# Performance work log

Measured on AMD Instinct MI355X. Metric: run time of the kernel, lower is better.

Reference implementation:

```python
import jax, jax.numpy as jnp
import numpy as np

H = 1152        # hidden_size
NH = 16         # num_heads
HD = H // NH    # head_dim = 72
MLP = int(H * 4.0)
EPS = 1e-6


def _ln(z, scale=None):
    # LayerNorm over last axis, eps=1e-6, no bias
    m = jnp.mean(z, axis=-1, keepdims=True)
    v = jnp.mean(jnp.square(z - m), axis=-1, keepdims=True)
    y = (z - m) * jax.lax.rsqrt(v + EPS)
    if scale is not None:
        y = y * scale
    return y


def setup_inputs() -> dict:
    key = jax.random.key(0)
    ks = jax.random.split(key, 16)
    B, N = 16, 1024
    x = jax.random.normal(ks[0], (B, N, H), dtype=jnp.float32)
    c = jax.random.normal(ks[1], (B, H), dtype=jnp.float32)
    def xav(k, fan_in, fan_out):
        lim = np.sqrt(6.0 / (fan_in + fan_out))
        return jax.random.uniform(k, (fan_in, fan_out), jnp.float32, -lim, lim)
    # adaLN modulation Dense (zero-init in original; use small random for a non-trivial test)
    w_mod = 0.02 * jax.random.normal(ks[2], (H, 6 * H), dtype=jnp.float32)
    b_mod = 0.02 * jax.random.normal(ks[3], (6 * H,), dtype=jnp.float32)
    w_qkv = xav(ks[4], H, 3 * H)
    b_qkv = jnp.zeros((3 * H,), jnp.float32)
    g_q = jnp.ones((HD,), jnp.float32)
    g_k = jnp.ones((HD,), jnp.float32)
    w_proj = xav(ks[5], H, H)
    b_proj = jnp.zeros((H,), jnp.float32)
    w1 = xav(ks[6], H, MLP)
    b1 = jnp.zeros((MLP,), jnp.float32)
    w2 = xav(ks[7], MLP, H)
    b2 = jnp.zeros((H,), jnp.float32)
    return dict(x=x, c=c, w_mod=w_mod, b_mod=b_mod, w_qkv=w_qkv, b_qkv=b_qkv,
                g_q=g_q, g_k=g_k, w_proj=w_proj, b_proj=b_proj,
                w1=w1, b1=b1, w2=w2, b2=b2)


def reference(x, c, w_mod, b_mod, w_qkv, b_qkv, g_q, g_k, w_proj, b_proj, w1, b1, w2, b2):
    B, N, _ = x.shape
    # adaLN-zero modulation from conditioning
    mod = jax.nn.swish(c) @ w_mod + b_mod                    # (B, 6H)
    sh_msa, sc_msa, g_msa, sh_mlp, sc_mlp, g_mlp = jnp.split(mod, 6, axis=1)
    # --- attention branch ---
    xn = _ln(x) * (1 + sc_msa[:, None, :]) + sh_msa[:, None, :]
    qkv = xn @ w_qkv + b_qkv                                 # (B, N, 3H)
    qkv = qkv.reshape(B, N, 3, NH, HD).transpose(2, 0, 3, 1, 4)
    q, k, v = qkv[0], qkv[1], qkv[2]                         # (B, NH, N, HD)
    q = _ln(q, g_q)
    k = _ln(k, g_k)
    attn = jax.nn.softmax(jnp.einsum('bhqd,bhkd->bhqk', q, k) * (HD ** -0.5), axis=-1)
    o = jnp.einsum('bhqk,bhkd->bhqd', attn, v)
    o = o.transpose(0, 2, 1, 3).reshape(B, N, H) @ w_proj + b_proj
    x = x + g_msa[:, None, :] * o
    # --- MLP branch ---
    xn2 = _ln(x) * (1 + sc_mlp[:, None, :]) + sh_mlp[:, None, :]
    h = jax.nn.gelu(xn2 @ w1 + b1, approximate=True)
    x = x + g_mlp[:, None, :] * (h @ w2 + b2)
    return x
```

## Files before the change

kernel.cpp:

```cpp
#include <hip/hip_runtime.h>
#include <hip/hip_bf16.h>

#define H     1152
#define H3    3456
#define H6    6912
#define NTOK  1024
#define NB    16
#define NHEAD 16
#define HDIM  72
#define MLPD  4608
#define ROWS  (NB*NTOK)
#define KSPLIT 16

typedef __hip_bfloat16 bf16;
typedef float f32x4 __attribute__((ext_vector_type(4)));
typedef __bf16 bf16x8 __attribute__((ext_vector_type(8)));
typedef const __attribute__((address_space(1))) void* gptr_as1;
typedef __attribute__((address_space(3))) void* lptr_as3;

__device__ __forceinline__ float b2f(bf16 v){ return __bfloat162float(v); }
__device__ __forceinline__ bf16  f2b(float v){ return __float2bfloat16(v); }
__device__ __forceinline__ unsigned short f2bu(float v){ return __builtin_bit_cast(unsigned short, __float2bfloat16(v)); }

template<int CTRL>
__device__ __forceinline__ float fdpp(float x) {
    int xi = __float_as_int(x);
    int r = __builtin_amdgcn_update_dpp(xi, xi, CTRL, 0xF, 0xF, true);
    return __int_as_float(r);
}
__device__ __forceinline__ float rowmax16(float x) {
    x = fmaxf(x, fdpp<0xB1>(x));
    x = fmaxf(x, fdpp<0x4E>(x));
    x = fmaxf(x, fdpp<0x141>(x));
    x = fmaxf(x, fdpp<0x140>(x));
    return x;
}
__device__ __forceinline__ float rowsum16(float x) {
    x += fdpp<0xB1>(x);
    x += fdpp<0x4E>(x);
    x += fdpp<0x141>(x);
    x += fdpp<0x140>(x);
    return x;
}

__global__ __launch_bounds__(256) void mod_partial_kernel(const float* __restrict__ c,
                                                          const float* __restrict__ w_mod,
                                                          float* __restrict__ partial) {
    const int ks = blockIdx.y;
    const int k0 = ks * (H/KSPLIT);
    __shared__ float sw[NB*(H/KSPLIT)];
    for (int i = threadIdx.x; i < NB*(H/KSPLIT); i += 256) {
        int b = i/(H/KSPLIT), k = i - b*(H/KSPLIT);
        float cv = c[b*H + k0 + k];
        sw[i] = cv / (1.f + __expf(-cv));
    }
    __syncthreads();
    const int col = blockIdx.x*256 + threadIdx.x;
    float acc[NB];
    #pragma unroll
    for (int b = 0; b < NB; ++b) acc[b] = 0.f;
    for (int k = 0; k < H/KSPLIT; ++k) {
        float wv = w_mod[(long)(k0+k)*H6 + col];
        #pragma unroll
        for (int b = 0; b < NB; ++b) acc[b] += sw[b*(H/KSPLIT)+k] * wv;
    }
    #pragma unroll
    for (int b = 0; b < NB; ++b) partial[((long)ks*NB + b)*H6 + col] = acc[b];
}

__global__ __launch_bounds__(256) void mod_reduce_kernel(const float* __restrict__ partial,
                                                         const float* __restrict__ b_mod,
                                                         float* __restrict__ mod) {
    const int idx = blockIdx.x*256 + threadIdx.x;
    const int col = idx % H6;
    float s = b_mod[col];
    #pragma unroll
    for (int ks = 0; ks < KSPLIT; ++ks) s += partial[(long)ks*NB*H6 + idx];
    mod[idx] = s;
}

__global__ __launch_bounds__(256) void ln_mod_kernel(const float* __restrict__ xin,
                                                     const float* __restrict__ mod,
                                                     int sh_off, int sc_off,
                                                     bf16* __restrict__ out,
                                                     int row0) {
    const int lrow = blockIdx.x;
    const long grow = (long)row0 + lrow;
    const int b = (int)(grow >> 10);
    const int tid = threadIdx.x;
    const long ibase = grow * H;
    const long obase = (long)lrow * H;
    __shared__ float sred[8];
    float vals[5];
    float sum = 0.f, sq = 0.f;
    #pragma unroll
    for (int i = 0; i < 5; ++i) {
        int cidx = i*256 + tid;
        float v = 0.f;
        if (cidx < H) v = xin[ibase+cidx];
        vals[i] = v; sum += v; sq += v*v;
    }
    #pragma unroll
    for (int off = 32; off > 0; off >>= 1) { sum += __shfl_down(sum, off); sq += __shfl_down(sq, off); }
    int wave = tid >> 6, lane = tid & 63;
    if (lane == 0) { sred[wave] = sum; sred[4+wave] = sq; }
    __syncthreads();
    if (tid == 0) {
        sred[0] = sred[0]+sred[1]+sred[2]+sred[3];
        sred[4] = sred[4]+sred[5]+sred[6]+sred[7];
    }
    __syncthreads();
    float mean = sred[0] * (1.f/H);
    float var  = sred[4] * (1.f/H) - mean*mean;
    float rstd = rsqrtf(var + 1e-6f);
    const float* mrow = mod + b*H6;
    #pragma unroll
    for (int i = 0; i < 5; ++i) {
        int cidx = i*256 + tid;
        if (cidx < H) {
            float y = (vals[i]-mean)*rstd;
            out[obase+cidx] = f2b(y * (1.f + mrow[sc_off+cidx]) + mrow[sh_off+cidx]);
        }
    }
}

__global__ __launch_bounds__(256) void transpose_kernel(const float* __restrict__ in,
                                                        bf16* __restrict__ out, int R, int C) {
    __shared__ bf16 tile[32][33];
    int c0 = blockIdx.x*32, r0 = blockIdx.y*32;
    int tx = threadIdx.x & 31, ty = threadIdx.x >> 5;
    for (int j = ty; j < 32; j += 8) tile[j][tx] = f2b(in[(long)(r0+j)*C + c0 + tx]);
    __syncthreads();
    for (int j = ty; j < 32; j += 8) out[(long)(c0+j)*R + r0 + tx] = tile[tx][j];
}

template<int EPI>
__global__ __launch_bounds__(256) void gemm_bt(const bf16* __restrict__ A, const bf16* __restrict__ BT,
                                               const float* __restrict__ bias,
                                               const float* __restrict__ res, const float* __restrict__ gate,
                                               bf16* __restrict__ C, float* __restrict__ Cf,
                                               int M, int N, int K, int row0) {
    __shared__ __align__(16) bf16 As[128*64];
    __shared__ __align__(16) bf16 Bs[128*64];
    const int tid  = threadIdx.x;
    const int wave = tid >> 6, lane = tid & 63;
    const int wm = wave & 1, wn = wave >> 1;
    const int col = lane & 15, quad = lane >> 4;
    f32x4 acc[4][4];
    #pragma unroll
    for (int i = 0; i < 4; ++i)
        #pragma unroll
        for (int j = 0; j < 4; ++j) acc[i][j] = (f32x4){0.f,0.f,0.f,0.f};

    const long arow0 = (long)blockIdx.y * 128;
    const long brow0 = (long)blockIdx.x * 128;
    const int  srow  = tid >> 3;
    const int  scol  = (tid & 7) * 8;
    const bf16* Ag = A + (arow0 + srow)*(long)K + scol;
    const bf16* Bg = BT + (brow0 + srow)*(long)K + scol;
    bf16* Asl = As + tid*8;
    bf16* Bsl = Bs + tid*8;

    for (int k0 = 0; k0 < K; k0 += 64) {
        __syncthreads();
        #pragma unroll
        for (int i = 0; i < 4; ++i) {
            __builtin_amdgcn_global_load_lds((gptr_as1)(Ag + (long)i*32*K + k0), (lptr_as3)(Asl + i*2048), 16, 0, 0);
            __builtin_amdgcn_global_load_lds((gptr_as1)(Bg + (long)i*32*K + k0), (lptr_as3)(Bsl + i*2048), 16, 0, 0);
        }
        __syncthreads();
        #pragma unroll
        for (int kk = 0; kk < 64; kk += 32) {
            bf16x8 af[4], bfr[4];
            #pragma unroll
            for (int mt = 0; mt < 4; ++mt) af[mt]  = *(const bf16x8*)&As[(wm*64+mt*16+col)*64 + kk + quad*8];
            #pragma unroll
            for (int nt = 0; nt < 4; ++nt) bfr[nt] = *(const bf16x8*)&Bs[(wn*64+nt*16+col)*64 + kk + quad*8];
            #pragma unroll
            for (int mt = 0; mt < 4; ++mt)
                #pragma unroll
                for (int nt = 0; nt < 4; ++nt)
                    acc[mt][nt] = __builtin_amdgcn_mfma_f32_16x16x32_bf16(af[mt], bfr[nt], acc[mt][nt], 0, 0, 0);
        }
    }

    #pragma unroll
    for (int mt = 0; mt < 4; ++mt) {
        #pragma unroll
        for (int nt = 0; nt < 4; ++nt) {
            const int colg = (int)brow0 + wn*64 + nt*16 + col;
            const float bv = bias[colg];
            #pragma unroll
            for (int r = 0; r < 4; ++r) {
                const long rowg = arow0 + wm*64 + mt*16 + quad*4 + r;
                float v = acc[mt][nt][r] + bv;
                if (EPI == 1) {
                    float u = 0.7978845608028654f*(v + 0.044715f*v*v*v);
                    v = v / (1.f + exp2f(-2.885390081777927f*u));
                    C[rowg*(long)N + colg] = f2b(v);
                } else if (EPI == 2) {
                    const long grow = row0 + rowg;
                    float g = gate[(int)(grow>>10)*H6 + colg];
                    Cf[grow*(long)N + colg] = res[grow*(long)N + colg] + g*v;
                } else {
                    C[rowg*(long)N + colg] = f2b(v);
                }
            }
        }
    }
}

__device__ __forceinline__ void ln72q(const bf16* __restrict__ src, const float* __restrict__ gw,
                                      float scale, bf16* __restrict__ dst, int lane) {
    const int i1 = 64 + (lane & 7);
    float e0 = b2f(src[lane]);
    float e1 = (lane < 8) ? b2f(src[i1]) : 0.f;
    float s = e0 + e1;
    #pragma unroll
    for (int off = 32; off > 0; off >>= 1) s += __shfl_xor(s, off);
    float mean = s * (1.f/72.f);
    float d0 = e0 - mean;
    float d1 = (lane < 8) ? (e1 - mean) : 0.f;
    float sq = d0*d0 + d1*d1;
    #pragma unroll
    for (int off = 32; off > 0; off >>= 1) sq += __shfl_xor(sq, off);
    float rstd = rsqrtf(sq*(1.f/72.f) + 1e-6f);
    dst[lane] = f2b(d0*rstd*gw[lane]*scale);
    if (lane < 32) {
        float y1 = (lane < 8) ? d1*rstd*gw[i1]*scale : 0.f;
        dst[64+lane] = f2b(y1);
    }
}

__device__ __forceinline__ void ln72k(const bf16* __restrict__ src, const float* __restrict__ gw,
                                      bf16* __restrict__ kb, int n, int lane) {
    const int i1 = 64 + (lane & 7);
    float e0 = b2f(src[lane]);
    float e1 = (lane < 8) ? b2f(src[i1]) : 0.f;
    float s = e0 + e1;
    #pragma unroll
    for (int off = 32; off > 0; off >>= 1) s += __shfl_xor(s, off);
    float mean = s * (1.f/72.f);
    float d0 = e0 - mean;
    float d1 = (lane < 8) ? (e1 - mean) : 0.f;
    float sq = d0*d0 + d1*d1;
    #pragma unroll
    for (int off = 32; off > 0; off >>= 1) sq += __shfl_xor(sq, off);
    float rstd = rsqrtf(sq*(1.f/72.f) + 1e-6f);
    const int kvb = n >> 4, nc = n & 15;
    {
        int off1 = ((kvb*3 + (lane>>5))<<9) + ((((lane&31)>>3)<<4) + nc)*8 + (lane&7);
        kb[off1] = f2b(d0*rstd*gw[lane]);
    }
    if (lane < 32) {
        float y1 = (lane < 8) ? d1*rstd*gw[i1] : 0.f;
        int off2 = ((kvb*3 + 2)<<9) + (((lane>>3)<<4) + nc)*8 + (lane&7);
        kb[off2] = f2b(y1);
    }
}

__global__ __launch_bounds__(256) void qk_ln_kernel(const bf16* __restrict__ qkv,
                                                    const float* __restrict__ g_q, const float* __restrict__ g_k,
                                                    bf16* __restrict__ qln, bf16* __restrict__ kln) {
    const int wave = threadIdx.x >> 6, lane = threadIdx.x & 63;
    const long g  = (long)blockIdx.x*4 + wave;
    const int  n  = (int)(g & 1023);
    const long bh = g >> 10;
    const int  h  = (int)(bh & 15);
    const int  b  = (int)(bh >> 4);
    const bf16* src = qkv + ((long)b*NTOK + n)*H3 + h*HDIM;
    ln72q(src,     g_q, 0.11785113019775793f * 1.4426950408889634f, qln + (bh*NTOK + n)*96, lane);
    ln72k(src + H, g_k, kln + bh*98304, n, lane);
}

__global__ __launch_bounds__(256) void v_transpose_kernel(const bf16* __restrict__ qkv, bf16* __restrict__ vt) {
    const int n0 = blockIdx.x*64;
    const int h = blockIdx.y, b = blockIdx.z;
    __shared__ bf16 tile[64][80];
    const long srcbase = ((long)b*NTOK + n0)*H3 + 2*H + h*HDIM;
    for (int idx = threadIdx.x; idx < 64*72; idx += 256) {
        int n = idx/72, d = idx - n*72;
        tile[n][d] = qkv[srcbase + (long)n*H3 + d];
    }
    for (int idx = threadIdx.x; idx < 64*8; idx += 256) {
        int n = idx >> 3, d = idx & 7;
        tile[n][72+d] = f2b(0.f);
    }
    __syncthreads();
    const long bh = (long)(b*NHEAD + h);
    bf16* dst = vt + (bh*16 + blockIdx.x)*5120;
    for (int o = threadIdx.x; o < 5120; o += 256) {
        int hv5 = o >> 9;
        int hv = (hv5 >= 5) ? 1 : 0;
        int nt = hv5 - hv*5;
        int lane = (o >> 3) & 63;
        int e = o & 7;
        int pos = hv*32 + ((lane>>4)<<3) + e;
        int kv_local = ((pos & 3) << 4) + (pos >> 2);
        int d = (nt << 4) + (lane & 15);
        dst[o] = tile[kv_local][d];
        (void)nt;
    }
}

#define PSTR 72
__global__ __launch_bounds__(512) void attn_kernel(const bf16* __restrict__ qln, const bf16* __restrict__ kln,
                                                   const bf16* __restrict__ vt, bf16* __restrict__ o,
                                                   int Bc) {
    const int tid = threadIdx.x;
    const int wave = tid >> 6, lane = tid & 63;
    const int qg = wave & 3, half = wave >> 2;
    const int col = lane & 15, quad = lane >> 4;

    const int L = blockIdx.x;
    const int P_ = 2*Bc;
    const int c8 = L & 7;
    const int j  = L >> 3;
    const int bh_l = c8*P_ + (j % P_);
    const int qt   = j / P_;
    const int b = bh_l >> 4, h = bh_l & 15;
    const long bh = bh_l;

    const int q0 = qt*64 + qg*16;
    const bf16* qb = qln + bh*NTOK*96;
    const bf16* kb = kln + bh*98304;
    const bf16* vb = vt  + bh*81920;

    __shared__ __align__(16) char smraw[28672];
    bf16* pw = (bf16*)smraw + wave*(16*PSTR);
    f32x4* Osm = (f32x4*)smraw;
    f32x4* Msm = (f32x4*)(smraw + 20480);
    f32x4* Lsm = (f32x4*)(smraw + 24576);

    bf16x8 qf[3];
    #pragma unroll
    for (int ks = 0; ks < 3; ++ks) qf[ks] = *(const bf16x8*)&qb[(q0+col)*96 + ks*32 + quad*8];

    f32x4 oacc[5];
    #pragma unroll
    for (int i = 0; i < 5; ++i) oacc[i] = (f32x4){0.f,0.f,0.f,0.f};
    float mrow[4], lrow[4];
    #pragma unroll
    for (int r = 0; r < 4; ++r) { mrow[r] = -1e30f; lrow[r] = 0.f; }

    const int kvbeg = half*512, kvend = kvbeg + 512;
    for (int kv0 = kvbeg; kv0 < kvend; kv0 += 64) {
        const int kvb16 = kv0 >> 4;
        const int kvt   = kv0 >> 6;
        f32x4 s[4];
        #pragma unroll
        for (int j4 = 0; j4 < 4; ++j4) s[j4] = (f32x4){0.f,0.f,0.f,0.f};
        #pragma unroll
        for (int j4 = 0; j4 < 4; ++j4)
            #pragma unroll
            for (int ks = 0; ks < 3; ++ks) {
                bf16x8 kf = *(const bf16x8*)&kb[(((kvb16 + j4)*3 + ks)<<9) + lane*8];
                s[j4] = __builtin_amdgcn_mfma_f32_16x16x32_bf16(qf[ks], kf, s[j4], 0, 0, 0);
            }
        float alpha[4];
        #pragma unroll
        for (int r = 0; r < 4; ++r) {
            float tm = fmaxf(fmaxf(s[0][r], s[1][r]), fmaxf(s[2][r], s[3][r]));
            tm = rowmax16(tm);
            float mn = fmaxf(mrow[r], tm);
            alpha[r] = exp2f(mrow[r] - mn);
            float p0 = exp2f(s[0][r] - mn);
            float p1 = exp2f(s[1][r] - mn);
            float p2 = exp2f(s[2][r] - mn);
            float p3 = exp2f(s[3][r] - mn);
            float ts = rowsum16((p0+p1)+(p2+p3));
            lrow[r] = lrow[r]*alpha[r] + ts;
            mrow[r] = mn;
            const int prow = quad*4 + r;
            unsigned int lo = (unsigned int)f2bu(p0) | ((unsigned int)f2bu(p1) << 16);
            unsigned int hi = (unsigned int)f2bu(p2) | ((unsigned int)f2bu(p3) << 16);
            unsigned long long pk = (unsigned long long)lo | ((unsigned long long)hi << 32);
            *(unsigned long long*)&pw[prow*PSTR + col*4] = pk;
        }
        if (__any(alpha[0]+alpha[1]+alpha[2]+alpha[3] < 4.f)) {
            #pragma unroll
            for (int i = 0; i < 5; ++i)
                #pragma unroll
                for (int r = 0; r < 4; ++r) oacc[i][r] *= alpha[r];
        }
        bf16x8 pf0 = *(const bf16x8*)&pw[col*PSTR + quad*8];
        bf16x8 pf1 = *(const bf16x8*)&pw[col*PSTR + 32 + quad*8];
        #pragma unroll
        for (int nt = 0; nt < 5; ++nt) {
            bf16x8 vf0 = *(const bf16x8*)&vb[((kvt*10 + nt)<<9) + lane*8];
            bf16x8 vf1 = *(const bf16x8*)&vb[((kvt*10 + 5 + nt)<<9) + lane*8];
            oacc[nt] = __builtin_amdgcn_mfma_f32_16x16x32_bf16(pf0, vf0, oacc[nt], 0, 0, 0);
            oacc[nt] = __builtin_amdgcn_mfma_f32_16x16x32_bf16(pf1, vf1, oacc[nt], 0, 0, 0);
        }
    }

    __syncthreads();
    if (half) {
        f32x4 mv, lv;
        #pragma unroll
        for (int r = 0; r < 4; ++r) { mv[r] = mrow[r]; lv[r] = lrow[r]; }
        Msm[qg*64 + lane] = mv;
        Lsm[qg*64 + lane] = lv;
        #pragma unroll
        for (int nt = 0; nt < 5; ++nt) Osm[(qg*5 + nt)*64 + lane] = oacc[nt];
    }
    __syncthreads();
    if (!half) {
        f32x4 mB = Msm[qg*64 + lane];
        f32x4 lB = Lsm[qg*64 + lane];
        float aA[4], aB[4], inv[4];
        #pragma unroll
        for (int r = 0; r < 4; ++r) {
            float ms = fmaxf(mrow[r], mB[r]);
            aA[r] = exp2f(mrow[r] - ms);
            aB[r] = exp2f(mB[r] - ms);
            float ls = lrow[r]*aA[r] + lB[r]*aB[r];
            inv[r] = 1.f / ls;
        }
        #pragma unroll
        for (int nt = 0; nt < 5; ++nt) {
            f32x4 oB = Osm[(qg*5 + nt)*64 + lane];
            int d = nt*16 + col;
            if (d < HDIM) {
                #pragma unroll
                for (int r = 0; r < 4; ++r) {
                    int qrow = q0 + quad*4 + r;
                    o[((long)b*NTOK + qrow)*H + h*HDIM + d] = f2b((oacc[nt][r]*aA[r] + oB[r]*aB[r])*inv[r]);
                }
            }
        }
    }
}

extern "C" void kernel_launch(void* const* d_in, const int* in_sizes, int n_in,
                              void* d_out, int out_size, void* d_ws, size_t ws_size,
                              hipStream_t stream) {
    const float* x      = (const float*)d_in[0];
    const float* c      = (const float*)d_in[1];
    const float* w_mod  = (const float*)d_in[2];
    const float* b_mod  = (const float*)d_in[3];
    const float* w_qkv  = (const float*)d_in[4];
    const float* b_qkv  = (const float*)d_in[5];
    const float* g_q    = (const float*)d_in[6];
    const float* g_k    = (const float*)d_in[7];
    const float* w_proj = (const float*)d_in[8];
    const float* b_proj = (const float*)d_in[9];
    const float* w1     = (const float*)d_in[10];
    const float* b1     = (const float*)d_in[11];
    const float* w2     = (const float*)d_in[12];
    const float* b2     = (const float*)d_in[13];
    float* out = (float*)d_out;

    char* ws = (char*)d_ws;
    size_t off = 0;
    auto alloc = [&](size_t bytes) { void* p = ws + off; off += (bytes + 255) & ~(size_t)255; return p; };
    float* modb  = (float*)alloc((size_t)NB*H6*4);
    bf16* wqkvT  = (bf16*)alloc((size_t)H3*H*2);
    bf16* wprojT = (bf16*)alloc((size_t)H*H*2);
    bf16* w1T    = (bf16*)alloc((size_t)MLPD*H*2);
    bf16* w2T    = (bf16*)alloc((size_t)H*MLPD*2);
    const size_t pers = off;

    int nchunk = 4;
    while (nchunk < 16 && pers + (size_t)(ROWS/nchunk)*(9216+8704) > ws_size) nchunk <<= 1;
    const int Rc = ROWS / nchunk;
    const int Bc = NB / nchunk;

    char* R1 = ws + pers;
    char* R2 = R1 + (size_t)Rc*9216;
    bf16* qkvc = (bf16*)R1;
    bf16* oc   = (bf16*)R1;
    bf16* hc   = (bf16*)R1;
    bf16* xnc  = (bf16*)R2;
    bf16* qlnc = (bf16*)R2;
    bf16* klnc = (bf16*)(R2 + (size_t)Rc*3072);
    bf16* vtc  = (bf16*)(R2 + (size_t)Rc*6144);
    float* modp = (float*)R1;

    mod_partial_kernel<<<dim3(H6/256, KSPLIT), 256, 0, stream>>>(c, w_mod, modp);
    mod_reduce_kernel<<<dim3(NB*H6/256), 256, 0, stream>>>(modp, b_mod, modb);
    transpose_kernel<<<dim3(H3/32,  H/32),   256, 0, stream>>>(w_qkv,  wqkvT,  H,    H3);
    transpose_kernel<<<dim3(H/32,   H/32),   256, 0, stream>>>(w_proj, wprojT, H,    H);
    transpose_kernel<<<dim3(MLPD/32,H/32),   256, 0, stream>>>(w1,     w1T,    H,    MLPD);
    transpose_kernel<<<dim3(H/32,   MLPD/32),256, 0, stream>>>(w2,     w2T,    MLPD, H);

    for (int ci = 0; ci < nchunk; ++ci) {
        const int row0 = ci * Rc;
        ln_mod_kernel<<<dim3(Rc), 256, 0, stream>>>(x, modb, 0, H, xnc, row0);
        gemm_bt<0><<<dim3(H3/128, Rc/128), 256, 0, stream>>>(xnc, wqkvT, b_qkv, nullptr, nullptr, qkvc, nullptr, Rc, H3, H, 0);
        qk_ln_kernel<<<dim3(Bc*NHEAD*NTOK/4), 256, 0, stream>>>(qkvc, g_q, g_k, qlnc, klnc);
        v_transpose_kernel<<<dim3(NTOK/64, NHEAD, Bc), 256, 0, stream>>>(qkvc, vtc);
        attn_kernel<<<dim3(256*Bc), 512, 0, stream>>>(qlnc, klnc, vtc, oc, Bc);
        gemm_bt<2><<<dim3(H/128, Rc/128), 256, 0, stream>>>(oc, wprojT, b_proj, x, modb + 2*H, nullptr, out, Rc, H, H, row0);
        ln_mod_kernel<<<dim3(Rc), 256, 0, stream>>>(out, modb, 3*H, 4*H, xnc, row0);
        gemm_bt<1><<<dim3(MLPD/128, Rc/128), 256, 0, stream>>>(xnc, w1T, b1, nullptr, nullptr, hc, nullptr, Rc, MLPD, H, 0);
        gemm_bt<2><<<dim3(H/128, Rc/128), 256, 0, stream>>>(hc, w2T, b2, out, modb + 5*H, nullptr, out, Rc, H, MLPD, row0);
    }
}
```

Before: 1.880 ms.

## Swizzle GEMM LDS tiles, remap blocks across XCDs, and default to one chunk

The GEMM now reads global memory with an XOR-swizzled column offset so that LDS fragment reads avoid bank conflicts. It also launches a 1D grid that is remapped so consecutive tiles are grouped per XCD (when the block count is a multiple of 8), which should improve L2 reuse. The attention block-index mapping is simplified to fixed shifts, and the chunk count now starts at 1, so the whole batch runs per launch when the workspace is large enough. Processing the batch in one pass needs a much larger workspace, and the fixed attention mapping assumes the per-chunk layout divides cleanly.

```diff
diff --git a/kernel.cpp b/kernel.cpp
--- a/kernel.cpp
+++ b/kernel.cpp
@@ -146,18 +146,26 @@
     const int wave = tid >> 6, lane = tid & 63;
     const int wm = wave & 1, wn = wave >> 1;
     const int col = lane & 15, quad = lane >> 4;
+
+    const int nbx = N >> 7;
+    const int nwg = gridDim.x;
+    const int L = blockIdx.x;
+    const int l = ((nwg & 7) == 0) ? ((L & 7)*(nwg >> 3) + (L >> 3)) : L;
+    const int bx = l % nbx, by = l / nbx;
+
     f32x4 acc[4][4];
     #pragma unroll
     for (int i = 0; i < 4; ++i)
         #pragma unroll
         for (int j = 0; j < 4; ++j) acc[i][j] = (f32x4){0.f,0.f,0.f,0.f};
 
-    const long arow0 = (long)blockIdx.y * 128;
-    const long brow0 = (long)blockIdx.x * 128;
+    const long arow0 = (long)by * 128;
+    const long brow0 = (long)bx * 128;
     const int  srow  = tid >> 3;
     const int  scol  = (tid & 7) * 8;
-    const bf16* Ag = A + (arow0 + srow)*(long)K + scol;
-    const bf16* Bg = BT + (brow0 + srow)*(long)K + scol;
+    const int  scolsw = scol ^ ((srow & 7) * 8);
+    const bf16* Ag = A + (arow0 + srow)*(long)K + scolsw;
+    const bf16* Bg = BT + (brow0 + srow)*(long)K + scolsw;
     bf16* Asl = As + tid*8;
     bf16* Bsl = Bs + tid*8;
 
@@ -169,13 +177,14 @@
             __builtin_amdgcn_global_load_lds((gptr_as1)(Bg + (long)i*32*K + k0), (lptr_as3)(Bsl + i*2048), 16, 0, 0);
         }
         __syncthreads();
+        const int xr = (col & 7) * 8;
         #pragma unroll
         for (int kk = 0; kk < 64; kk += 32) {
             bf16x8 af[4], bfr[4];
             #pragma unroll
-            for (int mt = 0; mt < 4; ++mt) af[mt]  = *(const bf16x8*)&As[(wm*64+mt*16+col)*64 + kk + quad*8];
+            for (int mt = 0; mt < 4; ++mt) af[mt]  = *(const bf16x8*)&As[(wm*64+mt*16+col)*64 + ((kk + quad*8) ^ xr)];
             #pragma unroll
-            for (int nt = 0; nt < 4; ++nt) bfr[nt] = *(const bf16x8*)&Bs[(wn*64+nt*16+col)*64 + kk + quad*8];
+            for (int nt = 0; nt < 4; ++nt) bfr[nt] = *(const bf16x8*)&Bs[(wn*64+nt*16+col)*64 + ((kk + quad*8) ^ xr)];
             #pragma unroll
             for (int mt = 0; mt < 4; ++mt)
                 #pragma unroll
@@ -313,11 +322,11 @@
     const int col = lane & 15, quad = lane >> 4;
 
     const int L = blockIdx.x;
-    const int P_ = 2*Bc;
     const int c8 = L & 7;
     const int j  = L >> 3;
-    const int bh_l = c8*P_ + (j % P_);
-    const int qt   = j / P_;
+    const int qt  = j & 15;
+    const int bhi = j >> 4;
+    const int bh_l = c8*(2*Bc) + bhi;
     const int b = bh_l >> 4, h = bh_l & 15;
     const long bh = bh_l;
 
@@ -461,7 +470,7 @@
     bf16* w2T    = (bf16*)alloc((size_t)H*MLPD*2);
     const size_t pers = off;
 
-    int nchunk = 4;
+    int nchunk = 1;
     while (nchunk < 16 && pers + (size_t)(ROWS/nchunk)*(9216+8704) > ws_size) nchunk <<= 1;
     const int Rc = ROWS / nchunk;
     const int Bc = NB / nchunk;
@@ -487,13 +496,13 @@
     for (int ci = 0; ci < nchunk; ++ci) {
         const int row0 = ci * Rc;
         ln_mod_kernel<<<dim3(Rc), 256, 0, stream>>>(x, modb, 0, H, xnc, row0);
-        gemm_bt<0><<<dim3(H3/128, Rc/128), 256, 0, stream>>>(xnc, wqkvT, b_qkv, nullptr, nullptr, qkvc, nullptr, Rc, H3, H, 0);
+        gemm_bt<0><<<dim3((H3/128)*(Rc/128)), 256, 0, stream>>>(xnc, wqkvT, b_qkv, nullptr, nullptr, qkvc, nullptr, Rc, H3, H, 0);
         qk_ln_kernel<<<dim3(Bc*NHEAD*NTOK/4), 256, 0, stream>>>(qkvc, g_q, g_k, qlnc, klnc);
         v_transpose_kernel<<<dim3(NTOK/64, NHEAD, Bc), 256, 0, stream>>>(qkvc, vtc);
         attn_kernel<<<dim3(256*Bc), 512, 0, stream>>>(qlnc, klnc, vtc, oc, Bc);
-        gemm_bt<2><<<dim3(H/128, Rc/128), 256, 0, stream>>>(oc, wprojT, b_proj, x, modb + 2*H, nullptr, out, Rc, H, H, row0);
+        gemm_bt<2><<<dim3((H/128)*(Rc/128)), 256, 0, stream>>>(oc, wprojT, b_proj, x, modb + 2*H, nullptr, out, Rc, H, H, row0);
         ln_mod_kernel<<<dim3(Rc), 256, 0, stream>>>(out, modb, 3*H, 4*H, xnc, row0);
-        gemm_bt<1><<<dim3(MLPD/128, Rc/128), 256, 0, stream>>>(xnc, w1T, b1, nullptr, nullptr, hc, nullptr, Rc, MLPD, H, 0);
-        gemm_bt<2><<<dim3(H/128, Rc/128), 256, 0, stream>>>(hc, w2T, b2, out, modb + 5*H, nullptr, out, Rc, H, MLPD, row0);
-    }
-}
+        gemm_bt<1><<<dim3((MLPD/128)*(Rc/128)), 256, 0, stream>>>(xnc, w1T, b1, nullptr, nullptr, hc, nullptr, Rc, MLPD, H, 0);
+        gemm_bt<2><<<dim3((H/128)*(Rc/128)), 256, 0, stream>>>(hc, w2T, b2, out, modb + 5*H, nullptr, out, Rc, H, MLPD, row0);
+    }
+}
```

Measured after the change: 1.557 ms. 17.2% less time.
